# Kernel optimization log

Hardware: AMD Instinct MI355X
Metric: run time of the kernel (lower is better)

## Reference

```python
import jax, jax.numpy as jnp
import numpy as np

NUM_HEADS = 8
GROUPS = 32
EPS = 1e-5


def setup_inputs() -> dict:
    key = jax.random.key(0)
    k1, k2, k3 = jax.random.split(key, 3)
    B, C, H, W = 16, 512, 64, 64
    x = jax.random.normal(k1, (B, C, H, W), dtype=jnp.float32)
    scale = C ** -0.5  # keep qkv/proj outputs well-scaled
    return {
        "x": x,
        "norm_w": jnp.ones((C,), jnp.float32),
        "norm_b": jnp.zeros((C,), jnp.float32),
        "qkv_w": jax.random.normal(k2, (3 * C, C), dtype=jnp.float32) * scale,
        "qkv_b": jnp.zeros((3 * C,), jnp.float32),
        "proj_w": jax.random.normal(k3, (C, C), dtype=jnp.float32) * scale,
        "proj_b": jnp.zeros((C,), jnp.float32),
    }


def reference(x, norm_w, norm_b, qkv_w, qkv_b, proj_w, proj_b):
    B, C, H, W = x.shape
    N = H * W
    nh = NUM_HEADS
    hd = C // nh

    # GroupNorm(32, C)
    xg = x.reshape(B, GROUPS, C // GROUPS, N)
    mu = xg.mean(axis=(2, 3), keepdims=True)
    var = xg.var(axis=(2, 3), keepdims=True)
    h = ((xg - mu) * jax.lax.rsqrt(var + EPS)).reshape(B, C, N)
    h = h * norm_w[None, :, None] + norm_b[None, :, None]

    h = h.transpose(0, 2, 1)  # [B, N, C]
    qkv = (h @ qkv_w.T + qkv_b).reshape(B, N, 3, nh, hd)
    q, k, v = qkv[:, :, 0], qkv[:, :, 1], qkv[:, :, 2]  # each [B, N, nh, hd]

    # Faithful to source: attention over the HEAD axis at each position
    attn = jnp.einsum('bnhd,bngd->bnhg', q, k) * (hd ** -0.5)  # [B, N, nh, nh]
    attn = jax.nn.softmax(attn, axis=-1)
    o = jnp.einsum('bnhg,bngd->bnhd', attn, v).reshape(B, N, C)

    o = o @ proj_w.T + proj_b  # [B, N, C]
    return x + o.transpose(0, 2, 1).reshape(B, C, H, W)
```

## Files before the change

kernel.cpp:

```cpp
#include <hip/hip_runtime.h>

typedef __attribute__((ext_vector_type(8))) short short8v;
typedef __attribute__((ext_vector_type(4))) float float4v;
typedef unsigned short ushortT;

__device__ __forceinline__ unsigned short f2bf(float f) {
  union { float f; unsigned u; } a; a.f = f;
  unsigned r = a.u + 0x7fffu + ((a.u >> 16) & 1u);
  return (unsigned short)(r >> 16);
}
__device__ __forceinline__ float2 up2(unsigned u) {
  union { unsigned u; float f; } a, b;
  a.u = u << 16; b.u = u & 0xffff0000u;
  return make_float2(a.f, b.f);
}
__device__ __forceinline__ void gl_lds16(const void* g, void* l) {
  __builtin_amdgcn_global_load_lds(
      (const __attribute__((address_space(1))) void*)g,
      (__attribute__((address_space(3))) void*)l, 16, 0, 0);
}

#define WAITV4 asm volatile("s_waitcnt vmcnt(4)" ::: "memory")
#define WAITV0 asm volatile("s_waitcnt vmcnt(0)" ::: "memory")
#define LGKM0  asm volatile("s_waitcnt lgkmcnt(0)" ::: "memory")
#define BAR()  __builtin_amdgcn_s_barrier()
#define MFMA16(d, a, b) d = __builtin_amdgcn_mfma_f32_16x16x32_bf16(a, b, d, 0, 0, 0)

__global__ __launch_bounds__(256) void wconv(const float* __restrict__ src,
                                             ushortT* __restrict__ dst, int n) {
  int i = (blockIdx.x * 256 + threadIdx.x) * 4;
  if (i < n) {
    float4 v = *(const float4*)(src + i);
    uint2 o;
    o.x = (unsigned)f2bf(v.x) | ((unsigned)f2bf(v.y) << 16);
    o.y = (unsigned)f2bf(v.z) | ((unsigned)f2bf(v.w) << 16);
    *(uint2*)(dst + i) = o;
  }
}

__global__ __launch_bounds__(256) void gn_stats(const float* __restrict__ x,
                                                float2* __restrict__ stats) {
  int bg = blockIdx.x;
  const float* base = x + (size_t)bg * 65536;
  int tid = threadIdx.x;
  float s = 0.f, s2 = 0.f;
  for (int i = tid; i < 16384; i += 256) {
    float4 v = *(const float4*)(base + (size_t)i * 4);
    s  += v.x + v.y + v.z + v.w;
    s2 += v.x * v.x + v.y * v.y + v.z * v.z + v.w * v.w;
  }
  #pragma unroll
  for (int off = 32; off > 0; off >>= 1) {
    s  += __shfl_down(s, off);
    s2 += __shfl_down(s2, off);
  }
  __shared__ float red[8];
  int w = tid >> 6, l = tid & 63;
  if (l == 0) { red[w] = s; red[w + 4] = s2; }
  __syncthreads();
  if (tid == 0) {
    float ts = red[0] + red[1] + red[2] + red[3];
    float t2 = red[4] + red[5] + red[6] + red[7];
    float mean = ts * (1.f / 65536.f);
    float var  = t2 * (1.f / 65536.f) - mean * mean;
    stats[bg] = make_float2(mean, rsqrtf(var + 1e-5f));
  }
}

__global__ __launch_bounds__(512) void norm_tr(const float* __restrict__ x,
                                               const float* __restrict__ nw,
                                               const float* __restrict__ nb,
                                               const float2* __restrict__ stats,
                                               ushortT* __restrict__ h) {
  __shared__ float t[64][65];
  int n0 = blockIdx.x * 64, c0 = blockIdx.y * 64, b = blockIdx.z;
  int tx = threadIdx.x, ty = threadIdx.y;
  #pragma unroll
  for (int j = ty; j < 64; j += 8) {
    int c = c0 + j;
    float2 ms = stats[b * 32 + (c >> 4)];
    float v = x[((size_t)b * 512 + c) * 4096 + n0 + tx];
    t[j][tx] = (v - ms.x) * ms.y * nw[c] + nb[c];
  }
  __syncthreads();
  #pragma unroll
  for (int j = ty; j < 64; j += 8) {
    int n = n0 + j;
    h[((size_t)b * 4096 + n) * 512 + c0 + tx] = f2bf(t[tx][j]);
  }
}

__device__ __forceinline__ void core256(const ushortT* __restrict__ A,
                                        const ushortT* __restrict__ Bm,
                                        ushortT* lds, int m0, int n0,
                                        float4v (&acc)[8][4]) {
  char* ldsb = (char*)lds;
  const int tid = threadIdx.x;
  const int w = tid >> 6, l = tid & 63;
  const int wm = w >> 2, wn = w & 3;

  const int P0b = tid * 16, P1b = 8192 + tid * 16;
  const int r0 = P0b >> 7, r1 = P1b >> 7;
  const int s0 = (P0b & 127) ^ ((r0 & 7) << 4);
  const int s1 = (P1b & 127) ^ ((r1 & 7) << 4);
  const size_t g0 = (size_t)r0 * 512 + (s0 >> 1);
  const size_t g1 = (size_t)r1 * 512 + (s1 >> 1);
  auto stage = [&](const ushortT* mat, int rowbase, int kt, int bufb, int region) {
    const ushortT* gsrc = mat + (size_t)rowbase * 512 + kt * 64;
    char* dbase = ldsb + bufb + region;
    gl_lds16(gsrc + g0, dbase + P0b);
    gl_lds16(gsrc + g1, dbase + P1b);
  };

  const int colb = (l >> 4) * 16;
  const int cs0 = colb ^ ((l & 7) << 4);
  const int cs1 = (64 + colb) ^ ((l & 7) << 4);
  const int arow = wm * 16384 + (l & 15) * 128;
  const int brow = 32768 + wn * 8192 + (l & 15) * 128;

  short8v Af[4][2], Bf[4][2];
  auto rdA = [&](int bb, int m, int mhalf) {
    const char* p = ldsb + bb + arow + m * 2048;
    Af[m][0] = *(const short8v*)(p + cs0);
    Af[m][1] = *(const short8v*)(p + cs1);
    (void)mhalf;
  };
  auto rdB = [&](int bb, int n) {
    const char* p = ldsb + bb + brow + n * 2048;
    Bf[n][0] = *(const short8v*)(p + cs0);
    Bf[n][1] = *(const short8v*)(p + cs1);
  };

  #define CLUSTER(MH, NP)                                              \
    { __builtin_amdgcn_s_setprio(1);                                   \
      _Pragma("unroll")                                                \
      for (int mm = 0; mm < 4; ++mm) {                                 \
        _Pragma("unroll")                                              \
        for (int nn = 0; nn < 2; ++nn) {                               \
          MFMA16(acc[(MH)*4+mm][(NP)*2+nn], Af[mm][0], Bf[(NP)*2+nn][0]); \
          MFMA16(acc[(MH)*4+mm][(NP)*2+nn], Af[mm][1], Bf[(NP)*2+nn][1]); \
        } }                                                            \
      __builtin_amdgcn_s_setprio(0); }

  auto tile = [&](int bb, int t1, int t2, bool s1g, bool s2g, int vw) {
    rdA(bb, 0, 0); rdA(bb, 1, 0); rdA(bb, 2, 0); rdA(bb, 3, 0);
    rdB(bb, 0); rdB(bb, 1);
    if (s1g) stage(A, m0 + 128, t1, bb ^ 65536, 16384);
    BAR(); LGKM0;
    CLUSTER(0, 0);
    BAR();
    rdB(bb, 2); rdB(bb, 3);
    if (s1g) stage(Bm, n0 + 128, t1, bb ^ 65536, 49152);
    BAR(); LGKM0;
    CLUSTER(0, 1);
    BAR();
    rdA(bb, 0, 1); rdA(bb, 1, 1); rdA(bb, 2, 1); rdA(bb, 3, 1);
    if (s2g) stage(Bm, n0, t2, bb, 32768);
    BAR(); LGKM0;
    CLUSTER(1, 1);
    BAR();
    if (s2g) stage(A, m0, t2, bb, 0);
    if (vw == 4)      { WAITV4; }
    else if (vw == 0) { WAITV0; }
    BAR();
    CLUSTER(1, 0);
    BAR();
  };
  #undef CLUSTER


  stage(A,  m0,       0, 0, 0);
  stage(A,  m0 + 128, 0, 0, 16384);
  stage(Bm, n0,       0, 0, 32768);
  stage(Bm, n0 + 128, 0, 0, 49152);
  stage(Bm, n0,       1, 65536, 32768);
  stage(A,  m0,       1, 65536, 0);
  WAITV4;
  BAR();

  #pragma unroll 1
  for (int tp = 0; tp < 3; ++tp) {
    int ta = 2 * tp, tb = 2 * tp + 1;
    tile(0,     ta + 1, ta + 2, true, true, 4);
    tile(65536, tb + 1, tb + 2, true, true, 4);
  }
  tile(0,     7, 8, true,  false, 0);
  tile(65536, 8, 9, false, false, -1);
}


__device__ __forceinline__ void core256b(const ushortT* __restrict__ A,
                                         const ushortT* __restrict__ Bm,
                                         ushortT* lds, int m0, int n0,
                                         float4v (&acc)[8][4]) {
  char* ldsb = (char*)lds;
  const int tid = threadIdx.x;
  const int w = tid >> 6, l = tid & 63;
  const int wm = w >> 2, wn = w & 3;

  const int P0b = tid * 16, P1b = 8192 + tid * 16;
  const int r0 = P0b >> 7, r1 = P1b >> 7;
  const int s0 = (P0b & 127) ^ ((r0 & 7) << 4);
  const int s1 = (P1b & 127) ^ ((r1 & 7) << 4);
  const size_t g0 = (size_t)r0 * 512 + (s0 >> 1);
  const size_t g1 = (size_t)r1 * 512 + (s1 >> 1);
  auto stage = [&](const ushortT* mat, int rowbase, int kt, int bufb, int region) {
    const ushortT* gsrc = mat + (size_t)rowbase * 512 + kt * 64;
    char* dbase = ldsb + bufb + region;
    gl_lds16(gsrc + g0, dbase + P0b);
    gl_lds16(gsrc + g1, dbase + P1b);
  };

  const int colb = (l >> 4) * 16;
  const int cs0 = colb ^ ((l & 7) << 4);
  const int cs1 = (64 + colb) ^ ((l & 7) << 4);
  const int arow = wm * 16384 + (l & 15) * 128;
  const int brow = 32768 + wn * 8192 + (l & 15) * 128;

  short8v Af[4][2], Bf[4][2];

  #define RDA4(bb, MH)                                                  \
    { _Pragma("unroll")                                                 \
      for (int mm = 0; mm < 4; ++mm) {                                  \
        const char* p = ldsb + (bb) + arow + ((MH)*4 + mm) * 2048;      \
        Af[mm][0] = *(const short8v*)(p + cs0);                         \
        Af[mm][1] = *(const short8v*)(p + cs1);                         \
      } }
  #define RDB2(bb, N0)                                                  \
    { _Pragma("unroll")                                                 \
      for (int nn = 0; nn < 2; ++nn) {                                  \
        const char* p = ldsb + (bb) + brow + ((N0) + nn) * 2048;        \
        Bf[(N0)+nn][0] = *(const short8v*)(p + cs0);                    \
        Bf[(N0)+nn][1] = *(const short8v*)(p + cs1);                    \
      } }
  #define CLUSTER(MH, NP)                                               \
    { __builtin_amdgcn_s_setprio(1);                                    \
      _Pragma("unroll")                                                 \
      for (int mm = 0; mm < 4; ++mm) {                                  \
        _Pragma("unroll")                                               \
        for (int nn = 0; nn < 2; ++nn) {                                \
          MFMA16(acc[(MH)*4+mm][(NP)*2+nn], Af[mm][0], Bf[(NP)*2+nn][0]); \
          MFMA16(acc[(MH)*4+mm][(NP)*2+nn], Af[mm][1], Bf[(NP)*2+nn][1]); \
        } }                                                             \
      __builtin_amdgcn_s_setprio(0); }

  auto tile = [&](int bb, int t1, int t2, bool s1g, bool s2g, int vw) {
    RDA4(bb, 0); RDB2(bb, 0);
    if (s1g) stage(A, m0 + 128, t1, bb ^ 65536, 16384);
    BAR(); LGKM0;
    CLUSTER(0, 0);
    BAR();
    RDB2(bb, 2);
    if (s1g) stage(Bm, n0 + 128, t1, bb ^ 65536, 49152);
    BAR(); LGKM0;
    CLUSTER(0, 1);
    BAR();
    RDA4(bb, 1);
    if (s2g) stage(Bm, n0, t2, bb, 32768);
    BAR(); LGKM0;
    CLUSTER(1, 1);
    BAR();
    if (s2g) stage(A, m0, t2, bb, 0);
    if (vw == 4)      { WAITV4; }
    else if (vw == 0) { WAITV0; }
    BAR();
    CLUSTER(1, 0);
    BAR();
  };

  stage(A,  m0,       0, 0, 0);
  stage(A,  m0 + 128, 0, 0, 16384);
  stage(Bm, n0,       0, 0, 32768);
  stage(Bm, n0 + 128, 0, 0, 49152);
  stage(Bm, n0,       1, 65536, 32768);
  stage(A,  m0,       1, 65536, 0);
  WAITV4;
  BAR();

  #pragma unroll 1
  for (int tp = 0; tp < 3; ++tp) {
    tile(0,     2 * tp + 1, 2 * tp + 2, true, true, 4);
    tile(65536, 2 * tp + 2, 2 * tp + 3, true, true, 4);
  }
  tile(0,     7, 8, true,  false, 0);
  tile(65536, 8, 9, false, false, -1);
  #undef RDA4
  #undef RDB2
  #undef CLUSTER
}

__global__ __launch_bounds__(512, 2) void gemm_qkv(const ushortT* __restrict__ h,
                                                   const ushortT* __restrict__ wq,
                                                   const float* __restrict__ bias,
                                                   ushortT* __restrict__ outq) {
  __shared__ ushortT lds[65536];
  int bid = blockIdx.x;
  int wg = (bid & 7) * 192 + (bid >> 3);
  int m0 = (wg / 6) * 256, n0 = (wg % 6) * 256;
  float4v acc[8][4] = {};
  core256b(h, wq, lds, m0, n0, acc);
  const int tid = threadIdx.x;
  const int w = tid >> 6, l = tid & 63;
  const int wm = w >> 2, wn = w & 3;
  __syncthreads();
  ushortT* es = lds + w * 1280;
  float bb[4];
  #pragma unroll
  for (int fn = 0; fn < 4; ++fn) bb[fn] = bias[n0 + wn * 64 + fn * 16 + (l & 15)];
  int r = l >> 2, g = l & 3;
  #pragma unroll
  for (int fm = 0; fm < 8; ++fm) {
    #pragma unroll
    for (int fn = 0; fn < 4; ++fn)
      #pragma unroll
      for (int j = 0; j < 4; ++j)
        es[((l >> 4) * 4 + j) * 72 + fn * 16 + (l & 15)] = f2bf(acc[fm][fn][j] + bb[fn]);
    uint4 v0 = *(const uint4*)(es + r * 72 + g * 16);
    uint4 v1 = *(const uint4*)(es + r * 72 + g * 16 + 8);
    size_t mrow = (size_t)m0 + wm * 128 + fm * 16 + r;
    uint4* dst = (uint4*)(outq + mrow * 1536 + n0 + wn * 64 + g * 16);
    dst[0] = v0; dst[1] = v1;
  }
}

__global__ __launch_bounds__(256) void attn_k(const ushortT* __restrict__ qkv,
                                              ushortT* __restrict__ o) {
  int gp = blockIdx.x * 256 + threadIdx.x;
  int pos = gp >> 3, hh = gp & 7;
  const ushortT* base = qkv + (size_t)pos * 1536;
  float q[64];
  #pragma unroll
  for (int i = 0; i < 8; ++i) {
    uint4 u = *(const uint4*)(base + hh * 64 + i * 8);
    float2 t0 = up2(u.x), t1 = up2(u.y), t2 = up2(u.z), t3 = up2(u.w);
    q[i*8+0]=t0.x; q[i*8+1]=t0.y; q[i*8+2]=t1.x; q[i*8+3]=t1.y;
    q[i*8+4]=t2.x; q[i*8+5]=t2.y; q[i*8+6]=t3.x; q[i*8+7]=t3.y;
  }
  float lg[8];
  #pragma unroll
  for (int g = 0; g < 8; ++g) {
    float s = 0.f;
    #pragma unroll
    for (int d8 = 0; d8 < 8; ++d8) {
      uint4 kk = *(const uint4*)(base + 512 + g * 64 + d8 * 8);
      float2 k0 = up2(kk.x), k1 = up2(kk.y), k2 = up2(kk.z), k3 = up2(kk.w);
      s += q[d8*8+0]*k0.x + q[d8*8+1]*k0.y + q[d8*8+2]*k1.x + q[d8*8+3]*k1.y
         + q[d8*8+4]*k2.x + q[d8*8+5]*k2.y + q[d8*8+6]*k3.x + q[d8*8+7]*k3.y;
    }
    lg[g] = s * 0.125f;
  }
  float mx = lg[0];
  #pragma unroll
  for (int g = 1; g < 8; ++g) mx = fmaxf(mx, lg[g]);
  float ssum = 0.f;
  #pragma unroll
  for (int g = 0; g < 8; ++g) { lg[g] = __expf(lg[g] - mx); ssum += lg[g]; }
  float inv = 1.f / ssum;
  #pragma unroll
  for (int g = 0; g < 8; ++g) lg[g] *= inv;
  float oa[64];
  #pragma unroll
  for (int i = 0; i < 64; ++i) oa[i] = 0.f;
  #pragma unroll
  for (int g = 0; g < 8; ++g) {
    float wg = lg[g];
    #pragma unroll
    for (int d8 = 0; d8 < 8; ++d8) {
      uint4 vv = *(const uint4*)(base + 1024 + g * 64 + d8 * 8);
      float2 v0 = up2(vv.x), v1 = up2(vv.y), v2 = up2(vv.z), v3 = up2(vv.w);
      oa[d8*8+0] += wg*v0.x; oa[d8*8+1] += wg*v0.y;
      oa[d8*8+2] += wg*v1.x; oa[d8*8+3] += wg*v1.y;
      oa[d8*8+4] += wg*v2.x; oa[d8*8+5] += wg*v2.y;
      oa[d8*8+6] += wg*v3.x; oa[d8*8+7] += wg*v3.y;
    }
  }
  ushortT* dst = o + (size_t)pos * 512 + hh * 64;
  #pragma unroll
  for (int i = 0; i < 8; ++i) {
    uint4 w_;
    w_.x = (unsigned)f2bf(oa[i*8+0]) | ((unsigned)f2bf(oa[i*8+1]) << 16);
    w_.y = (unsigned)f2bf(oa[i*8+2]) | ((unsigned)f2bf(oa[i*8+3]) << 16);
    w_.z = (unsigned)f2bf(oa[i*8+4]) | ((unsigned)f2bf(oa[i*8+5]) << 16);
    w_.w = (unsigned)f2bf(oa[i*8+6]) | ((unsigned)f2bf(oa[i*8+7]) << 16);
    *(uint4*)(dst + i * 8) = w_;
  }
}

__global__ __launch_bounds__(512, 2) void gemm_proj(const ushortT* __restrict__ o,
                                                    const ushortT* __restrict__ wp,
                                                    const float* __restrict__ bias,
                                                    const float* __restrict__ x,
                                                    float* __restrict__ out) {
  __shared__ ushortT lds[65536];
  int bid = blockIdx.x;
  int wg = (bid & 7) * 64 + (bid >> 3);
  int m0 = (wg >> 1) * 256, n0 = (wg & 1) * 256;
  float4v acc[8][4] = {};
  core256b(o, wp, lds, m0, n0, acc);
  const int tid = threadIdx.x;
  const int w = tid >> 6, l = tid & 63;
  const int wm = w >> 2, wn = w & 3;
  __syncthreads();
  float* es = (float*)((char*)lds + w * 4608);
  int b = m0 >> 12;
  int c = n0 + wn * 64 + l;
  float bc = bias[c];
  const float* xrow = x + ((size_t)b * 512 + c) * 4096;
  float* orow = out + ((size_t)b * 512 + c) * 4096;
  int nb0 = (m0 & 4095) + wm * 128;
  #pragma unroll
  for (int fm = 0; fm < 8; ++fm) {
    #pragma unroll
    for (int fn = 0; fn < 4; ++fn)
      #pragma unroll
      for (int j = 0; j < 4; ++j)
        es[((l >> 4) * 4 + j) * 68 + fn * 16 + (l & 15)] = acc[fm][fn][j];
    int nb = nb0 + fm * 16;
    #pragma unroll
    for (int q4 = 0; q4 < 4; ++q4) {
      float4 xv = *(const float4*)(xrow + nb + q4 * 4);
      float4 ov;
      ov.x = xv.x + bc + es[(q4 * 4 + 0) * 68 + l];
      ov.y = xv.y + bc + es[(q4 * 4 + 1) * 68 + l];
      ov.z = xv.z + bc + es[(q4 * 4 + 2) * 68 + l];
      ov.w = xv.w + bc + es[(q4 * 4 + 3) * 68 + l];
      *(float4*)(orow + nb + q4 * 4) = ov;
    }
  }
}

extern "C" void kernel_launch(void* const* d_in, const int* in_sizes, int n_in,
                              void* d_out, int out_size, void* d_ws, size_t ws_size,
                              hipStream_t stream) {
  const float* x     = (const float*)d_in[0];
  const float* nw    = (const float*)d_in[1];
  const float* nb    = (const float*)d_in[2];
  const float* qkvw  = (const float*)d_in[3];
  const float* qkvb  = (const float*)d_in[4];
  const float* pw    = (const float*)d_in[5];
  const float* pb    = (const float*)d_in[6];
  float* out = (float*)d_out;
  char* ws = (char*)d_ws;

  const size_t OFF_WQ   = 4096;
  const size_t OFF_WP   = OFF_WQ + 1572864;
  const size_t OFF_H    = OFF_WP + 524288;
  const size_t OFF_QKV  = OFF_H + 67108864;

  float2* stats   = (float2*)ws;
  ushortT* wq_b   = (ushortT*)(ws + OFF_WQ);
  ushortT* wp_b   = (ushortT*)(ws + OFF_WP);
  ushortT* h      = (ushortT*)(ws + OFF_H);
  ushortT* qkv    = (ushortT*)(ws + OFF_QKV);

  wconv<<<768, 256, 0, stream>>>(qkvw, wq_b, 786432);
  wconv<<<256, 256, 0, stream>>>(pw,   wp_b, 262144);
  gn_stats<<<512, 256, 0, stream>>>(x, stats);
  norm_tr<<<dim3(64, 8, 16), dim3(64, 8), 0, stream>>>(x, nw, nb, stats, h);
  gemm_qkv<<<1536, 512, 0, stream>>>(h, wq_b, qkvb, qkv);
  attn_k<<<2048, 256, 0, stream>>>(qkv, h);
  gemm_proj<<<512, 512, 0, stream>>>(h, wp_b, pb, x, out);
}
```

Baseline: 406.7 us.

## Merge weight conversion and GroupNorm stats into one prep kernel; drop explicit LDS waits

Combines the two weight-conversion launches and the GroupNorm statistics launch into a single prep kernel that dispatches on block index, saving two kernel launches and their gaps. It also removes the explicit lgkmcnt(0) waits in the GEMM tile loop and reorders the B/A fragment reads, leaving the compiler to insert the LDS waits, which could allow more overlap. The unused core256 function is deleted. Relying on compiler-inserted waits around barriers risks either extra conservative waits or subtler scheduling changes.

```diff
diff --git a/kernel.cpp b/kernel.cpp
--- a/kernel.cpp
+++ b/kernel.cpp
@@ -22,27 +22,30 @@
 
 #define WAITV4 asm volatile("s_waitcnt vmcnt(4)" ::: "memory")
 #define WAITV0 asm volatile("s_waitcnt vmcnt(0)" ::: "memory")
-#define LGKM0  asm volatile("s_waitcnt lgkmcnt(0)" ::: "memory")
 #define BAR()  __builtin_amdgcn_s_barrier()
 #define MFMA16(d, a, b) d = __builtin_amdgcn_mfma_f32_16x16x32_bf16(a, b, d, 0, 0, 0)
 
-__global__ __launch_bounds__(256) void wconv(const float* __restrict__ src,
-                                             ushortT* __restrict__ dst, int n) {
-  int i = (blockIdx.x * 256 + threadIdx.x) * 4;
-  if (i < n) {
+__global__ __launch_bounds__(256) void prep(const float* __restrict__ qkvw,
+                                            const float* __restrict__ pw,
+                                            const float* __restrict__ x,
+                                            ushortT* __restrict__ wq_b,
+                                            ushortT* __restrict__ wp_b,
+                                            float2* __restrict__ stats) {
+  int bid = blockIdx.x, tid = threadIdx.x;
+  if (bid < 1024) {
+    const float* src = (bid < 768) ? qkvw : pw;
+    ushortT* dst     = (bid < 768) ? wq_b : wp_b;
+    int base = (bid < 768) ? bid : (bid - 768);
+    int i = (base * 256 + tid) * 4;
     float4 v = *(const float4*)(src + i);
     uint2 o;
     o.x = (unsigned)f2bf(v.x) | ((unsigned)f2bf(v.y) << 16);
     o.y = (unsigned)f2bf(v.z) | ((unsigned)f2bf(v.w) << 16);
     *(uint2*)(dst + i) = o;
-  }
-}
-
-__global__ __launch_bounds__(256) void gn_stats(const float* __restrict__ x,
-                                                float2* __restrict__ stats) {
-  int bg = blockIdx.x;
+    return;
+  }
+  int bg = bid - 1024;
   const float* base = x + (size_t)bg * 65536;
-  int tid = threadIdx.x;
   float s = 0.f, s2 = 0.f;
   for (int i = tid; i < 16384; i += 256) {
     float4 v = *(const float4*)(base + (size_t)i * 4);
@@ -89,105 +92,6 @@
     h[((size_t)b * 4096 + n) * 512 + c0 + tx] = f2bf(t[tx][j]);
   }
 }
-
-__device__ __forceinline__ void core256(const ushortT* __restrict__ A,
-                                        const ushortT* __restrict__ Bm,
-                                        ushortT* lds, int m0, int n0,
-                                        float4v (&acc)[8][4]) {
-  char* ldsb = (char*)lds;
-  const int tid = threadIdx.x;
-  const int w = tid >> 6, l = tid & 63;
-  const int wm = w >> 2, wn = w & 3;
-
-  const int P0b = tid * 16, P1b = 8192 + tid * 16;
-  const int r0 = P0b >> 7, r1 = P1b >> 7;
-  const int s0 = (P0b & 127) ^ ((r0 & 7) << 4);
-  const int s1 = (P1b & 127) ^ ((r1 & 7) << 4);
-  const size_t g0 = (size_t)r0 * 512 + (s0 >> 1);
-  const size_t g1 = (size_t)r1 * 512 + (s1 >> 1);
-  auto stage = [&](const ushortT* mat, int rowbase, int kt, int bufb, int region) {
-    const ushortT* gsrc = mat + (size_t)rowbase * 512 + kt * 64;
-    char* dbase = ldsb + bufb + region;
-    gl_lds16(gsrc + g0, dbase + P0b);
-    gl_lds16(gsrc + g1, dbase + P1b);
-  };
-
-  const int colb = (l >> 4) * 16;
-  const int cs0 = colb ^ ((l & 7) << 4);
-  const int cs1 = (64 + colb) ^ ((l & 7) << 4);
-  const int arow = wm * 16384 + (l & 15) * 128;
-  const int brow = 32768 + wn * 8192 + (l & 15) * 128;
-
-  short8v Af[4][2], Bf[4][2];
-  auto rdA = [&](int bb, int m, int mhalf) {
-    const char* p = ldsb + bb + arow + m * 2048;
-    Af[m][0] = *(const short8v*)(p + cs0);
-    Af[m][1] = *(const short8v*)(p + cs1);
-    (void)mhalf;
-  };
-  auto rdB = [&](int bb, int n) {
-    const char* p = ldsb + bb + brow + n * 2048;
-    Bf[n][0] = *(const short8v*)(p + cs0);
-    Bf[n][1] = *(const short8v*)(p + cs1);
-  };
-
-  #define CLUSTER(MH, NP)                                              \
-    { __builtin_amdgcn_s_setprio(1);                                   \
-      _Pragma("unroll")                                                \
-      for (int mm = 0; mm < 4; ++mm) {                                 \
-        _Pragma("unroll")                                              \
-        for (int nn = 0; nn < 2; ++nn) {                               \
-          MFMA16(acc[(MH)*4+mm][(NP)*2+nn], Af[mm][0], Bf[(NP)*2+nn][0]); \
-          MFMA16(acc[(MH)*4+mm][(NP)*2+nn], Af[mm][1], Bf[(NP)*2+nn][1]); \
-        } }                                                            \
-      __builtin_amdgcn_s_setprio(0); }
-
-  auto tile = [&](int bb, int t1, int t2, bool s1g, bool s2g, int vw) {
-    rdA(bb, 0, 0); rdA(bb, 1, 0); rdA(bb, 2, 0); rdA(bb, 3, 0);
-    rdB(bb, 0); rdB(bb, 1);
-    if (s1g) stage(A, m0 + 128, t1, bb ^ 65536, 16384);
-    BAR(); LGKM0;
-    CLUSTER(0, 0);
-    BAR();
-    rdB(bb, 2); rdB(bb, 3);
-    if (s1g) stage(Bm, n0 + 128, t1, bb ^ 65536, 49152);
-    BAR(); LGKM0;
-    CLUSTER(0, 1);
-    BAR();
-    rdA(bb, 0, 1); rdA(bb, 1, 1); rdA(bb, 2, 1); rdA(bb, 3, 1);
-    if (s2g) stage(Bm, n0, t2, bb, 32768);
-    BAR(); LGKM0;
-    CLUSTER(1, 1);
-    BAR();
-    if (s2g) stage(A, m0, t2, bb, 0);
-    if (vw == 4)      { WAITV4; }
-    else if (vw == 0) { WAITV0; }
-    BAR();
-    CLUSTER(1, 0);
-    BAR();
-  };
-  #undef CLUSTER
-
-
-  stage(A,  m0,       0, 0, 0);
-  stage(A,  m0 + 128, 0, 0, 16384);
-  stage(Bm, n0,       0, 0, 32768);
-  stage(Bm, n0 + 128, 0, 0, 49152);
-  stage(Bm, n0,       1, 65536, 32768);
-  stage(A,  m0,       1, 65536, 0);
-  WAITV4;
-  BAR();
-
-  #pragma unroll 1
-  for (int tp = 0; tp < 3; ++tp) {
-    int ta = 2 * tp, tb = 2 * tp + 1;
-    tile(0,     ta + 1, ta + 2, true, true, 4);
-    tile(65536, tb + 1, tb + 2, true, true, 4);
-  }
-  tile(0,     7, 8, true,  false, 0);
-  tile(65536, 8, 9, false, false, -1);
-}
-
 
 __device__ __forceinline__ void core256b(const ushortT* __restrict__ A,
                                          const ushortT* __restrict__ Bm,
@@ -245,19 +149,19 @@
       __builtin_amdgcn_s_setprio(0); }
 
   auto tile = [&](int bb, int t1, int t2, bool s1g, bool s2g, int vw) {
-    RDA4(bb, 0); RDB2(bb, 0);
+    RDB2(bb, 0); RDA4(bb, 0);
     if (s1g) stage(A, m0 + 128, t1, bb ^ 65536, 16384);
-    BAR(); LGKM0;
+    BAR();
     CLUSTER(0, 0);
     BAR();
     RDB2(bb, 2);
     if (s1g) stage(Bm, n0 + 128, t1, bb ^ 65536, 49152);
-    BAR(); LGKM0;
+    BAR();
     CLUSTER(0, 1);
     BAR();
     RDA4(bb, 1);
     if (s2g) stage(Bm, n0, t2, bb, 32768);
-    BAR(); LGKM0;
+    BAR();
     CLUSTER(1, 1);
     BAR();
     if (s2g) stage(A, m0, t2, bb, 0);
@@ -453,9 +357,7 @@
   ushortT* h      = (ushortT*)(ws + OFF_H);
   ushortT* qkv    = (ushortT*)(ws + OFF_QKV);
 
-  wconv<<<768, 256, 0, stream>>>(qkvw, wq_b, 786432);
-  wconv<<<256, 256, 0, stream>>>(pw,   wp_b, 262144);
-  gn_stats<<<512, 256, 0, stream>>>(x, stats);
+  prep<<<1536, 256, 0, stream>>>(qkvw, pw, x, wq_b, wp_b, stats);
   norm_tr<<<dim3(64, 8, 16), dim3(64, 8), 0, stream>>>(x, nw, nb, stats, h);
   gemm_qkv<<<1536, 512, 0, stream>>>(h, wq_b, qkvb, qkv);
   attn_k<<<2048, 256, 0, stream>>>(qkv, h);
```

New measurement: 397.7 us. -2.2%, faster.
